# Performance work log

Measured on AMD Instinct MI355X. Metric: run time of the kernel, lower is better.

Reference implementation:

```python
import jax, jax.numpy as jnp
import numpy as np

D, H, F, Z = 768, 12, 2048, 100   # d_model, nhead, dim_feedforward, d_z
NL = 2                            # num enc layers == num dec layers
RATIO = 0.05                      # filter_ratio
EPS = 1e-5


def _ln(x, g, b):
    m = x.mean(-1, keepdims=True)
    v = ((x - m) ** 2).mean(-1, keepdims=True)
    return (x - m) / jnp.sqrt(v + EPS) * g + b


def _mha(x, bias, qkv_w, qkv_b, out_w, out_b):
    # x: [N, L, D] (torch seq-first: seq=N responses, batch=L token positions)
    # bias: [L, N] float key-padding mask, ADDED to logits (torch float-mask semantics)
    N, L, _ = x.shape
    hd = D // H
    qkv = jnp.einsum('nld,ed->nle', x, qkv_w) + qkv_b
    q, k, v = jnp.split(qkv, 3, axis=-1)
    q = q.reshape(N, L, H, hd)
    k = k.reshape(N, L, H, hd)
    v = v.reshape(N, L, H, hd)
    scores = jnp.einsum('nlhd,mlhd->lhnm', q, k) / jnp.sqrt(jnp.float32(hd))
    scores = scores + bias[:, None, None, :]
    attn = jax.nn.softmax(scores, axis=-1)
    o = jnp.einsum('lhnm,mlhd->nlhd', attn, v).reshape(N, L, D)
    return o @ out_w.T + out_b


def _stack(x, bias, p):
    qkv_w, qkv_b, out_w, out_b, g1, b1, w1, c1, w2, c2, g2, b2 = p
    for i in range(NL):  # post-norm TransformerEncoderLayer, relu FFN, eval (no dropout)
        a = _mha(x, bias, qkv_w[i], qkv_b[i], out_w[i], out_b[i])
        x = _ln(x + a, g1[i], b1[i])
        f = jax.nn.relu(x @ w1[i].T + c1[i]) @ w2[i].T + c2[i]
        x = _ln(x + f, g2[i], b2[i])
    return x


def _anomaly_scores(emb, msk, enc_p, dec_p, pe_w, pe_b, pd_w, pd_b):
    bias = msk.T  # [L, N]
    h = _stack(emb, bias, enc_p)
    z = jnp.tanh(h @ pe_w.T + pe_b)
    zd = jnp.tanh(z @ pd_w.T + pd_b)
    d = _stack(zd, bias, dec_p)
    # per-response MSE between mean decoded and mean input embedding, summed over D
    return ((d.mean(axis=1) - emb.mean(axis=1)) ** 2).sum(-1)


def _forward(tree_lens, inputs_embeds, attention_mask, enc_p, dec_p, pe_w, pe_b, pd_w, pd_b):
    B, T, L, _ = inputs_embeds.shape
    tls = np.asarray(tree_lens)
    n_resp = tls - 1
    # pack ragged replies: rows 1..tree_len-1 of every tree -> [Ntot, L, D]
    b_idx = np.concatenate([np.full(n, b) for b, n in enumerate(n_resp)])
    t_idx = np.concatenate([np.arange(1, tl) for tl in tls])
    reply = inputs_embeds[b_idx, t_idx]
    masks = attention_mask[b_idx, t_idx]
    s = _anomaly_scores(reply, masks, enc_p, dec_p, pe_w, pe_b, pd_w, pd_b)  # [Ntot]
    Ntot = s.shape[0]
    # original: rank_idx = global_argsort filtered to indices < n_resp[b] (min is always 0)
    # == argsort of the FIRST n_resp[b] packed scores (faithful to the source's indexing)
    masked = jnp.where(jnp.arange(Ntot)[None, :] < jnp.asarray(n_resp)[:, None],
                       s[None, :], jnp.inf)
    order = jnp.argsort(masked, axis=1)[:, :T - 1]  # [B, T-1]
    n_ext = np.maximum(np.floor(n_resp * RATIO).astype(np.int64), 1)
    sel = np.arange(T - 1)[None, :] < n_ext[:, None]          # [B, T-1]
    selj = jnp.asarray(sel)
    node_idx = jnp.where(selj, order + 1, 0)                  # pad slots reuse src (node 0)
    node_full = jnp.concatenate([jnp.zeros((B, 1), node_idx.dtype), node_idx], axis=1)
    brow = jnp.arange(B)[:, None]
    new_emb = inputs_embeds[brow, node_full]                  # [B, T, L, D]
    valid = jnp.asarray(np.concatenate([np.ones((B, 1), bool), sel], axis=1)
                        ).astype(attention_mask.dtype)
    new_msk = attention_mask[brow, node_full] * valid[:, :, None]  # pad rows get zero mask
    ohidx = jnp.where(selj, order + 1, T)                     # dump masked scatters to col T
    oh = jnp.zeros((B, T + 1), jnp.int32).at[brow, ohidx].set(1)[:, :T].at[:, 0].set(1)
    ext_mask = jnp.repeat(oh[:, :, None], L, axis=2).reshape(B, T * L)
    new_tree_lens = jnp.asarray(1 + n_ext, dtype=jnp.int32)
    n_ext_adv = 0
    return oh, ext_mask, n_ext_adv, new_tree_lens, new_emb, new_msk


def setup_inputs() -> dict:
    B, T, L = 16, 32, 64
    key = jax.random.key(0)
    ks = list(jax.random.split(key, 4))
    inp = {
        'tree_lens': jax.random.randint(ks[0], (B,), T // 2, T + 1),
        'inputs_embeds': jax.random.normal(ks[1], (B, T, L, D), jnp.float32),
        'attention_mask': jnp.ones((B, T, L), jnp.float32),
    }
    kit = iter(jax.random.split(ks[2], 32))
    def w(shape):
        return jax.random.normal(next(kit), (NL,) + shape, jnp.float32) * 0.02
    for pre in ('enc', 'dec'):
        inp[pre + '_qkv_w'] = w((3 * D, D)); inp[pre + '_qkv_b'] = jnp.zeros((NL, 3 * D))
        inp[pre + '_out_w'] = w((D, D));     inp[pre + '_out_b'] = jnp.zeros((NL, D))
        inp[pre + '_ln1_g'] = jnp.ones((NL, D)); inp[pre + '_ln1_b'] = jnp.zeros((NL, D))
        inp[pre + '_w1'] = w((F, D)); inp[pre + '_c1'] = jnp.zeros((NL, F))
        inp[pre + '_w2'] = w((D, F)); inp[pre + '_c2'] = jnp.zeros((NL, D))
        inp[pre + '_ln2_g'] = jnp.ones((NL, D)); inp[pre + '_ln2_b'] = jnp.zeros((NL, D))
    inp['pe_w'] = jax.random.normal(next(kit), (Z, D), jnp.float32) * 0.02
    inp['pe_b'] = jnp.zeros((Z,), jnp.float32)
    inp['pd_w'] = jax.random.normal(next(kit), (D, Z), jnp.float32) * 0.02
    inp['pd_b'] = jnp.zeros((D,), jnp.float32)
    return inp


def reference(tree_lens, inputs_embeds, attention_mask,
              enc_qkv_w, enc_qkv_b, enc_out_w, enc_out_b, enc_ln1_g, enc_ln1_b,
              enc_w1, enc_c1, enc_w2, enc_c2, enc_ln2_g, enc_ln2_b,
              dec_qkv_w, dec_qkv_b, dec_out_w, dec_out_b, dec_ln1_g, dec_ln1_b,
              dec_w1, dec_c1, dec_w2, dec_c2, dec_ln2_g, dec_ln2_b,
              pe_w, pe_b, pd_w, pd_b):
    enc_p = (enc_qkv_w, enc_qkv_b, enc_out_w, enc_out_b, enc_ln1_g, enc_ln1_b,
             enc_w1, enc_c1, enc_w2, enc_c2, enc_ln2_g, enc_ln2_b)
    dec_p = (dec_qkv_w, dec_qkv_b, dec_out_w, dec_out_b, dec_ln1_g, dec_ln1_b,
             dec_w1, dec_c1, dec_w2, dec_c2, dec_ln2_g, dec_ln2_b)
    return _forward(tree_lens, inputs_embeds, attention_mask, enc_p, dec_p,
                    pe_w, pe_b, pd_w, pd_b)
```

## Files before the change

kernel.cpp:

```cpp
#include <hip/hip_runtime.h>
#include <hip/hip_bf16.h>
#include <math.h>


#define B_  16
#define T_  32
#define L_  64
#define D_  768
#define H_  12
#define F_  2048
#define ZR_ 100
#define NP_ 512
#define EPS_ 1e-5f

#define MI_NTOT  0
#define MI_NRESP 8
#define MI_OFF   32
#define MI_BIDX  64
#define MI_TIDX  576
#define MI_NODE  1088

#define WS_BIAS2 2048
#define WS_EMEAN 34816
#define WS_S     428032
#define WS_WST   428544
#define WS_BIG   1313280

#define PEB_F    (WS_WST + 196608)

#define OUT_OH   0
#define OUT_EXT  512
#define OUT_NEA  33280
#define OUT_NTL  33281
#define OUT_NEMB 33297
#define OUT_NMSK 25199121
#define OUT_XSCR 33300
#define OUT_WSTK 12616224

#define WSEG0 1769472
#define WSEG1 589824
#define WSEG2 1572864
#define WSEG3 1572864
#define WPASS 5505024

typedef __attribute__((ext_vector_type(8))) short short8;
typedef __attribute__((ext_vector_type(4))) float f32x4;

__device__ inline float bf2f(unsigned s) {
  return __uint_as_float((s & 0xffffu) << 16);
}
__device__ inline unsigned short f2bf(float x) {
  unsigned u = __float_as_uint(x);
  u += 0x7fffu + ((u >> 16) & 1u);
  return (unsigned short)(u >> 16);
}
__device__ inline unsigned pack2(float a, float b) {
  return (unsigned)f2bf(a) | ((unsigned)f2bf(b) << 16);
}

__global__ void meta_kernel(const int* __restrict__ tl, int* __restrict__ mi) {
  if (threadIdx.x != 0) return;
  int off = 0;
  for (int b = 0; b < B_; b++) {
    int nr = tl[b] - 1;
    mi[MI_NRESP + b] = nr;
    mi[MI_OFF + b] = off;
    off += nr;
  }
  mi[MI_NTOT] = off;
  for (int j = 0; j < NP_; j++) {
    int b = -1, t = 0;
    if (j < off) {
      b = 0;
      while (b + 1 < B_ && j >= mi[MI_OFF + b + 1]) b++;
      t = j - mi[MI_OFF + b] + 1;
    }
    mi[MI_BIDX + j] = b;
    mi[MI_TIDX + j] = t;
  }
}

__global__ __launch_bounds__(256) void w2bf4_kernel(
    const float* __restrict__ s0, const float* __restrict__ s1,
    const float* __restrict__ s2, const float* __restrict__ s3,
    unsigned short* __restrict__ dst) {
  const int e = blockIdx.x * 1024 + threadIdx.x * 4;
  const float* src;
  int off;
  if (e < WSEG0)                         { src = s0; off = e; }
  else if (e < WSEG0 + WSEG1)            { src = s1; off = e - WSEG0; }
  else if (e < WSEG0 + WSEG1 + WSEG2)    { src = s2; off = e - WSEG0 - WSEG1; }
  else                                   { src = s3; off = e - WSEG0 - WSEG1 - WSEG2; }
  float4 v = *(const float4*)(src + off);
  uint2 pk; pk.x = pack2(v.x, v.y); pk.y = pack2(v.z, v.w);
  *(uint2*)(dst + e) = pk;
}

__global__ __launch_bounds__(256) void pepd_stage(
    const float* __restrict__ pew, const float* __restrict__ peb,
    const float* __restrict__ pdw,
    unsigned short* __restrict__ dpe, unsigned short* __restrict__ dpd,
    float* __restrict__ dpeb) {
  const int blk = blockIdx.x, t = threadIdx.x;
  if (blk < 192) {
    const int e = blk * 1024 + t * 4;
    const int r = e / 768, c = e % 768;
    float v[4];
    #pragma unroll
    for (int j = 0; j < 4; j++) v[j] = (r < ZR_) ? pew[r * 768 + c + j] : 0.f;
    uint2 pk; pk.x = pack2(v[0], v[1]); pk.y = pack2(v[2], v[3]);
    *(uint2*)(dpe + e) = pk;
  } else if (blk < 384) {
    const int e = (blk - 192) * 1024 + t * 4;
    const int r = e / 256, c = e % 256;
    float v[4];
    #pragma unroll
    for (int j = 0; j < 4; j++) v[j] = (c + j < ZR_) ? pdw[r * ZR_ + c + j] : 0.f;
    uint2 pk; pk.x = pack2(v[0], v[1]); pk.y = pack2(v[2], v[3]);
    *(uint2*)(dpd + e) = pk;
  } else {
    dpeb[t] = (t < ZR_) ? peb[t] : 0.f;
  }
}

__global__ __launch_bounds__(192) void gather_kernel(
    const float* __restrict__ emb, const float* __restrict__ am,
    const int* __restrict__ mi, unsigned short* __restrict__ X,
    float* __restrict__ bias2) {
  const int blk = blockIdx.x;
  const int j = blk >> 6, l = blk & 63;
  const int ntot = mi[MI_NTOT];
  const int t = threadIdx.x;
  float4 v = make_float4(0.f, 0.f, 0.f, 0.f);
  if (j < ntot) {
    const int b = mi[MI_BIDX + j], tt = mi[MI_TIDX + j];
    v = ((const float4*)(emb + (size_t)((b * T_ + tt) * L_ + l) * D_))[t];
    if (t == 0) bias2[blk] = am[(b * T_ + tt) * L_ + l];
  } else {
    if (t == 0) bias2[blk] = -1e30f;
  }
  uint2 pk; pk.x = pack2(v.x, v.y); pk.y = pack2(v.z, v.w);
  *(uint2*)(X + (size_t)blk * D_ + t * 4) = pk;
}

__global__ __launch_bounds__(256) void zerotail_kernel(const int* __restrict__ mi,
                                                       unsigned short* __restrict__ BIG) {
  const int row = blockIdx.x;
  if (row < mi[MI_NTOT] * 64) return;
  uint4 z = make_uint4(0u, 0u, 0u, 0u);
  uint4* p = (uint4*)(BIG + (size_t)row * 2304);
  for (int c = threadIdx.x; c < 288; c += 256) p[c] = z;
}

__global__ __launch_bounds__(256) void emean_kernel(const unsigned short* __restrict__ X,
                                                    float* __restrict__ em) {
  const int j = blockIdx.x;
  int d = threadIdx.x;
  for (int c = 0; c < 3; c++, d += 256) {
    const unsigned short* p = X + (size_t)j * L_ * D_ + d;
    float s = 0.f;
    for (int l = 0; l < L_; l++) s += bf2f(p[l * D_]);
    em[j * D_ + d] = s * (1.f / 64.f);
  }
}

__device__ inline float blockSum256(float v, float* red) {
  #pragma unroll
  for (int o = 32; o > 0; o >>= 1) v += __shfl_down(v, o);
  const int lane = threadIdx.x & 63, wid = threadIdx.x >> 6;
  __syncthreads();
  if (lane == 0) red[wid] = v;
  __syncthreads();
  return red[0] + red[1] + red[2] + red[3];
}

__global__ __launch_bounds__(256) void ln_kernel(unsigned short* __restrict__ X,
                                                 const float* __restrict__ g,
                                                 const float* __restrict__ bb,
                                                 const int* __restrict__ mi) {
  const int row = blockIdx.x;
  if (row >= mi[MI_NTOT] * L_) return;
  unsigned short* p = X + (size_t)row * D_;
  const int t = threadIdx.x;
  __shared__ float red[4];
  float v0 = bf2f(p[t]), v1 = bf2f(p[t + 256]), v2 = bf2f(p[t + 512]);
  float s = blockSum256(v0 + v1 + v2, red);
  float m = s * (1.f / 768.f);
  float d0 = v0 - m, d1 = v1 - m, d2 = v2 - m;
  float q = blockSum256(d0 * d0 + d1 * d1 + d2 * d2, red);
  float r = rsqrtf(q * (1.f / 768.f) + EPS_);
  p[t]       = f2bf(d0 * r * g[t]       + bb[t]);
  p[t + 256] = f2bf(d1 * r * g[t + 256] + bb[t + 256]);
  p[t + 512] = f2bf(d2 * r * g[t + 512] + bb[t + 512]);
}

template <int ACT, bool ADD>
__global__ __launch_bounds__(256, 2) void gemm_mfma(
    const unsigned short* __restrict__ A, int lda, int K,
    const unsigned short* __restrict__ W, int ldw,
    const float* __restrict__ bias,
    unsigned short* __restrict__ C, int ldc, int CT,
    const int* __restrict__ mi) {
  const int rows = mi[MI_NTOT] * 64;
  const int RTa = (rows + 255) >> 8;
  const int NTa = RTa * CT;
  const int id = blockIdx.x;
  if (id >= NTa) return;
  const int q8 = NTa >> 3, r8 = NTa & 7;
  const int xcd = id & 7, idx = id >> 3;
  const int wg = (xcd < r8 ? xcd * (q8 + 1) : r8 * (q8 + 1) + (xcd - r8) * q8) + idx;
  const int row0 = (wg / CT) * 256;
  const int col0 = (wg % CT) * 128;
  __shared__ unsigned short As[3][256 * 32];
  __shared__ unsigned short Bs[3][128 * 32];
  const int t = threadIdx.x;
  const int lane = t & 63, w = t >> 6;
  const int wr = w >> 1, wc = w & 1;
  const int quad = lane >> 4, l15 = lane & 15;

  const int srow = t >> 2;
  const int sgs = (t & 3) ^ ((t >> 3) & 3);
  const unsigned short* aSrc = A + (size_t)(row0 + srow) * lda + sgs * 8;
  const unsigned short* bSrc = W + (size_t)(col0 + srow) * ldw + sgs * 8;

#define STAGE_(kk, Ad, Bd)                                                      \
  do {                                                                          \
    __builtin_amdgcn_global_load_lds(                                           \
        (const __attribute__((address_space(1))) void*)(aSrc + (kk)),           \
        (__attribute__((address_space(3))) void*)((Ad) + w * 512), 16, 0, 0);   \
    __builtin_amdgcn_global_load_lds(                                           \
        (const __attribute__((address_space(1))) void*)(aSrc + (size_t)64 * lda + (kk)), \
        (__attribute__((address_space(3))) void*)((Ad) + 2048 + w * 512), 16, 0, 0); \
    __builtin_amdgcn_global_load_lds(                                           \
        (const __attribute__((address_space(1))) void*)(aSrc + (size_t)128 * lda + (kk)), \
        (__attribute__((address_space(3))) void*)((Ad) + 4096 + w * 512), 16, 0, 0); \
    __builtin_amdgcn_global_load_lds(                                           \
        (const __attribute__((address_space(1))) void*)(aSrc + (size_t)192 * lda + (kk)), \
        (__attribute__((address_space(3))) void*)((Ad) + 6144 + w * 512), 16, 0, 0); \
    __builtin_amdgcn_global_load_lds(                                           \
        (const __attribute__((address_space(1))) void*)(bSrc + (kk)),           \
        (__attribute__((address_space(3))) void*)((Bd) + w * 512), 16, 0, 0);   \
    __builtin_amdgcn_global_load_lds(                                           \
        (const __attribute__((address_space(1))) void*)(bSrc + (size_t)64 * ldw + (kk)), \
        (__attribute__((address_space(3))) void*)((Bd) + 2048 + w * 512), 16, 0, 0); \
  } while (0)

  auto LDA_ = [&](const unsigned short* buf, int m) -> short8 {
    const int ar = wr * 128 + m * 16 + l15;
    return *(const short8*)(buf + ar * 32 + (quad ^ ((ar >> 1) & 3)) * 8);
  };
  auto LDB_ = [&](const unsigned short* buf, int n) -> short8 {
    const int bn = wc * 64 + n * 16 + l15;
    return *(const short8*)(buf + bn * 32 + (quad ^ ((bn >> 1) & 3)) * 8);
  };

  f32x4 acc[8][4];
  #pragma unroll
  for (int m = 0; m < 8; m++)
    #pragma unroll
    for (int n = 0; n < 4; n++) acc[m][n] = (f32x4){0.f, 0.f, 0.f, 0.f};

  unsigned short* a0 = As[0]; unsigned short* a1 = As[1]; unsigned short* a2 = As[2];
  unsigned short* b0 = Bs[0]; unsigned short* b1 = Bs[1]; unsigned short* b2 = Bs[2];

  STAGE_(0, a0, b0);
  STAGE_(32, a1, b1);
  __builtin_amdgcn_sched_barrier(0);
  asm volatile("s_waitcnt vmcnt(6)" ::: "memory");
  __builtin_amdgcn_sched_barrier(0);
  __builtin_amdgcn_s_barrier();
  __builtin_amdgcn_sched_barrier(0);

  const int KT = K >> 5;
  for (int kt = 0; kt < KT; ++kt) {
    const bool m2 = (kt + 2) < KT;
    const int kn = (kt + 2) << 5;
    short8 afr[4], bfr[4];

    #pragma unroll
    for (int n = 0; n < 4; n++) bfr[n] = LDB_(b0, n);
    #pragma unroll
    for (int m = 0; m < 4; m++) afr[m] = LDA_(a0, m);
    if (m2) STAGE_(kn, a2, b2);
    __builtin_amdgcn_s_setprio(1);
    #pragma unroll
    for (int m = 0; m < 4; m++)
      #pragma unroll
      for (int n = 0; n < 4; n++)
        acc[m][n] = __builtin_amdgcn_mfma_f32_16x16x32_bf16(afr[m], bfr[n], acc[m][n], 0, 0, 0);
    __builtin_amdgcn_s_setprio(0);

    #pragma unroll
    for (int m = 0; m < 4; m++) afr[m] = LDA_(a0, m + 4);
    __builtin_amdgcn_s_setprio(1);
    #pragma unroll
    for (int m = 0; m < 4; m++)
      #pragma unroll
      for (int n = 0; n < 4; n++)
        acc[m + 4][n] = __builtin_amdgcn_mfma_f32_16x16x32_bf16(afr[m], bfr[n], acc[m + 4][n], 0, 0, 0);
    __builtin_amdgcn_s_setprio(0);

    if (kt + 1 < KT) {
      __builtin_amdgcn_sched_barrier(0);
      if (m2) asm volatile("s_waitcnt vmcnt(6)" ::: "memory");
      else    asm volatile("s_waitcnt vmcnt(0)" ::: "memory");
      __builtin_amdgcn_sched_barrier(0);
      __builtin_amdgcn_s_barrier();
      __builtin_amdgcn_sched_barrier(0);
    }
    unsigned short* ta = a0; a0 = a1; a1 = a2; a2 = ta;
    unsigned short* tb = b0; b0 = b1; b1 = b2; b2 = tb;
  }
#undef STAGE_

  float bv[4];
  #pragma unroll
  for (int n = 0; n < 4; n++) bv[n] = bias[col0 + wc * 64 + n * 16 + l15];
  #pragma unroll
  for (int m = 0; m < 8; m++) {
    #pragma unroll
    for (int reg = 0; reg < 4; reg++) {
      const size_t cr = (size_t)(row0 + wr * 128 + m * 16 + quad * 4 + reg) * ldc;
      #pragma unroll
      for (int n = 0; n < 4; n++) {
        const int cn = col0 + wc * 64 + n * 16 + l15;
        float x = acc[m][n][reg] + bv[n];
        if (ACT == 1) x = fmaxf(x, 0.f);
        if (ACT == 2) x = tanhf(x);
        if (ADD) x += bf2f(C[cr + cn]);
        C[cr + cn] = f2bf(x);
      }
    }
  }
}

__global__ __launch_bounds__(512) void attn_kernel(
    unsigned short* __restrict__ QKV, const float* __restrict__ bias2,
    const int* __restrict__ mi) {
  const int ntot = mi[MI_NTOT];
  const int id = blockIdx.x;
  const int xcd = id & 7, rr = id >> 3;
  const int ntp = rr & 3, lhi = rr >> 2;
  if (ntp * 128 >= ntot) return;
  const int lh = lhi * 8 + xcd;
  const int l = lh / H_, h = lh - l * H_;
  __shared__ unsigned short QPs[128 * 64];
  __shared__ unsigned short Ks0[64 * 64], Ks1[64 * 64];
  __shared__ unsigned short Vt0[64 * 64], Vt1[64 * 64];
  __shared__ float Bls[512];
  const int t = threadIdx.x;
  const int lane = t & 63, w = t >> 6;
  const int quad = lane >> 4, l15 = lane & 15;
  const int q0 = ntp * 128;
  const size_t TSTRIDE = (size_t)64 * L_ * 2304;

  const int krow = t >> 3;
  const int kgs = (t & 7) ^ (krow & 7);
  const unsigned short* ksrc =
      QKV + (size_t)(krow * L_ + l) * 2304 + 768 + h * 64 + kgs * 8;
  const unsigned short* vsrc =
      QKV + (size_t)(lane * L_ + l) * 2304 + 1536 + h * 64 + w * 8;

  auto stageK = [&](int mt, unsigned short* Kw) {
    __builtin_amdgcn_global_load_lds(
        (const __attribute__((address_space(1))) void*)(ksrc + (size_t)mt * TSTRIDE),
        (__attribute__((address_space(3))) void*)(Kw + w * 512), 16, 0, 0);
  };
  auto scatterV = [&](uint4 a0, unsigned short* Vw) {
    const unsigned short* p0 = (const unsigned short*)&a0;
    #pragma unroll
    for (int j = 0; j < 8; j++) {
      const int d = w * 8 + j;
      Vw[d * 64 + ((lane >> 3) ^ (d & 7)) * 8 + (lane & 7)] = p0[j];
    }
  };

  #pragma unroll
  for (int r = 0; r < 2; r++) {
    const int c = r * 512 + t;
    const int row = c >> 3, g = c & 7, gs = g ^ (row & 7);
    const unsigned short* gq =
        QKV + (size_t)((q0 + row) * L_ + l) * 2304 + h * 64 + gs * 8;
    __builtin_amdgcn_global_load_lds(
        (const __attribute__((address_space(1))) void*)gq,
        (__attribute__((address_space(3))) void*)(QPs + r * 4096 + w * 512), 16, 0, 0);
  }
  stageK(0, Ks0);
  uint4 pv0 = *(const uint4*)vsrc;
  Bls[t] = bias2[t * 64 + l];
  __syncthreads();

  const int qrow = w * 16 + l15;
  short8 aq[2];
  #pragma unroll
  for (int kq = 0; kq < 2; kq++)
    aq[kq] = *(const short8*)(QPs + qrow * 64 + ((kq * 4 + quad) ^ (qrow & 7)) * 8);
  scatterV(pv0, Vt0);
  __syncthreads();

  float runmax = -3.0e38f, runsum = 0.f;
  f32x4 oacc[4];
  #pragma unroll
  for (int i = 0; i < 4; i++) oacc[i] = (f32x4){0.f, 0.f, 0.f, 0.f};

  auto tilecomp = [&](int mt, const unsigned short* Krd, const unsigned short* Vrd) {
    f32x4 sa[4];
    #pragma unroll
    for (int n = 0; n < 4; n++) sa[n] = (f32x4){0.f, 0.f, 0.f, 0.f};
    __builtin_amdgcn_s_setprio(1);
    #pragma unroll
    for (int n = 0; n < 4; n++) {
      const int kr = n * 16 + l15;
      #pragma unroll
      for (int kq = 0; kq < 2; kq++) {
        const short8 bk = *(const short8*)(Krd + kr * 64 + ((kq * 4 + quad) ^ (kr & 7)) * 8);
        sa[n] = __builtin_amdgcn_mfma_f32_16x16x32_bf16(bk, aq[kq], sa[n], 0, 0, 0);
      }
    }
    __builtin_amdgcn_s_setprio(0);
    #pragma unroll
    for (int n = 0; n < 4; n++) {
      const float4 bj = *(const float4*)(Bls + mt * 64 + n * 16 + quad * 4);
      sa[n][0] = sa[n][0] * 0.125f + bj.x;
      sa[n][1] = sa[n][1] * 0.125f + bj.y;
      sa[n][2] = sa[n][2] * 0.125f + bj.z;
      sa[n][3] = sa[n][3] * 0.125f + bj.w;
    }

    float m16 = -3.0e38f;
    #pragma unroll
    for (int n = 0; n < 4; n++)
      m16 = fmaxf(m16, fmaxf(fmaxf(sa[n][0], sa[n][1]), fmaxf(sa[n][2], sa[n][3])));
    m16 = fmaxf(m16, __shfl_xor(m16, 16));
    m16 = fmaxf(m16, __shfl_xor(m16, 32));
    const float nm = fmaxf(runmax, m16);
    const float alpha = __expf(runmax - nm);
    runmax = nm;
    float s16 = 0.f;
    #pragma unroll
    for (int n = 0; n < 4; n++)
      #pragma unroll
      for (int reg = 0; reg < 4; reg++) {
        const float p = __expf(sa[n][reg] - nm);
        sa[n][reg] = p; s16 += p;
      }
    s16 += __shfl_xor(s16, 16);
    s16 += __shfl_xor(s16, 32);
    runsum = runsum * alpha + s16;
    float al[4];
    #pragma unroll
    for (int reg = 0; reg < 4; reg++)
      al[reg] = __shfl(alpha, (lane & 48) | (quad * 4 + reg));
    #pragma unroll
    for (int dn = 0; dn < 4; dn++)
      #pragma unroll
      for (int reg = 0; reg < 4; reg++) oacc[dn][reg] *= al[reg];

    #pragma unroll
    for (int n = 0; n < 4; n++)
      #pragma unroll
      for (int reg = 0; reg < 4; reg++) {
        const int key = n * 16 + quad * 4 + reg;
        QPs[qrow * 64 + ((key >> 3) ^ (qrow & 7)) * 8 + (key & 7)] = f2bf(sa[n][reg]);
      }
    short8 ap[2];
    #pragma unroll
    for (int kq = 0; kq < 2; kq++)
      ap[kq] = *(const short8*)(QPs + qrow * 64 + ((kq * 4 + quad) ^ (qrow & 7)) * 8);

    __builtin_amdgcn_s_setprio(1);
    #pragma unroll
    for (int dn = 0; dn < 4; dn++) {
      const int dr = dn * 16 + l15;
      #pragma unroll
      for (int kq = 0; kq < 2; kq++) {
        const short8 bv = *(const short8*)(Vrd + dr * 64 + ((kq * 4 + quad) ^ (dr & 7)) * 8);
        oacc[dn] = __builtin_amdgcn_mfma_f32_16x16x32_bf16(ap[kq], bv, oacc[dn], 0, 0, 0);
      }
    }
    __builtin_amdgcn_s_setprio(0);
  };

  for (int mt2 = 0; mt2 < 8; mt2 += 2) {
    {
      stageK(mt2 + 1, Ks1);
      uint4 n0 = *(const uint4*)(vsrc + (size_t)(mt2 + 1) * TSTRIDE);
      tilecomp(mt2, Ks0, Vt0);
      scatterV(n0, Vt1);
      __syncthreads();
    }
    {
      const bool more = (mt2 + 2) < 8;
      uint4 m0 = make_uint4(0, 0, 0, 0);
      if (more) {
        stageK(mt2 + 2, Ks0);
        m0 = *(const uint4*)(vsrc + (size_t)(mt2 + 2) * TSTRIDE);
      }
      tilecomp(mt2 + 1, Ks1, Vt1);
      if (more) scatterV(m0, Vt0);
      __syncthreads();
    }
  }

  const float inv = 1.f / runsum;
  float iv[4];
  #pragma unroll
  for (int reg = 0; reg < 4; reg++)
    iv[reg] = __shfl(inv, (lane & 48) | (quad * 4 + reg));
  #pragma unroll
  for (int reg = 0; reg < 4; reg++) {
    const int q = q0 + w * 16 + quad * 4 + reg;
    unsigned short* op = QKV + (size_t)(q * L_ + l) * 2304 + h * 64;
    #pragma unroll
    for (int dn = 0; dn < 4; dn++)
      op[dn * 16 + l15] = f2bf(oacc[dn][reg] * iv[reg]);
  }
}

__global__ __launch_bounds__(256) void score_kernel(const unsigned short* __restrict__ X,
                                                    const float* __restrict__ em,
                                                    float* __restrict__ Sv) {
  const int j = blockIdx.x;
  const int t = threadIdx.x;
  __shared__ float red[4];
  float part = 0.f;
  for (int c = 0; c < 3; c++) {
    const int d = t + c * 256;
    const unsigned short* p = X + (size_t)j * L_ * D_ + d;
    float s = 0.f;
    for (int l = 0; l < L_; l++) s += bf2f(p[l * D_]);
    const float diff = s * (1.f / 64.f) - em[j * D_ + d];
    part += diff * diff;
  }
  const float tot = blockSum256(part, red);
  if (t == 0) Sv[j] = tot;
}

__global__ __launch_bounds__(256) void finalize_kernel(const float* __restrict__ Sv,
                                                       int* __restrict__ mi,
                                                       float* __restrict__ out) {
  const int t = threadIdx.x;
  if (t < B_) {
    const int nr = mi[MI_NRESP + t];
    float best = 3.0e38f; int bi = 0;
    for (int j = 0; j < nr; j++) {
      const float v = Sv[j];
      if (v < best) { best = v; bi = j; }
    }
    mi[MI_NODE + t] = bi + 1;
    int next = nr / 20; if (next < 1) next = 1;
    out[OUT_NTL + t] = (float)(1 + next);
  }
  if (t == 0) out[OUT_NEA] = 0.f;
  __syncthreads();
  for (int idx = t; idx < B_ * T_; idx += 256) {
    const int b = idx >> 5, tt = idx & 31;
    out[OUT_OH + idx] = (tt == 0 || tt == mi[MI_NODE + b]) ? 1.f : 0.f;
  }
}

__global__ __launch_bounds__(256) void maskout_kernel(const float* __restrict__ am,
                                                      const int* __restrict__ mi,
                                                      float* __restrict__ out) {
  const int idx = blockIdx.x * 256 + threadIdx.x;
  const int b = idx >> 11, rem = idx & 2047;
  const int tt = rem >> 6, l = rem & 63;
  const int node = mi[MI_NODE + b];
  out[OUT_EXT + idx] = (tt == 0 || tt == node) ? 1.f : 0.f;
  float nm;
  if (tt == 0)      nm = am[(b * T_) * L_ + l];
  else if (tt == 1) nm = am[(b * T_ + node) * L_ + l];
  else              nm = 0.f;
  out[OUT_NMSK + idx] = nm;
}

__global__ __launch_bounds__(192) void newemb_kernel(const float* __restrict__ emb,
                                                     const int* __restrict__ mi,
                                                     float* __restrict__ out) {
  const int blk = blockIdx.x;
  const int b = blk >> 11, rem = blk & 2047;
  const int tt = rem >> 6, l = rem & 63;
  const int srct = (tt == 1) ? mi[MI_NODE + b] : 0;
  const float4 v = ((const float4*)(emb + (size_t)((b * T_ + srct) * L_ + l) * D_))[threadIdx.x];
  float* dst = out + OUT_NEMB + (size_t)blk * D_ + threadIdx.x * 4;
  dst[0] = v.x; dst[1] = v.y; dst[2] = v.z; dst[3] = v.w;
}

extern "C" void kernel_launch(void* const* d_in, const int* in_sizes, int n_in,
                              void* d_out, int out_size, void* d_ws, size_t ws_size,
                              hipStream_t stream) {
  (void)in_sizes; (void)n_in; (void)out_size; (void)ws_size;
  const int*   tl  = (const int*)d_in[0];
  const float* emb = (const float*)d_in[1];
  const float* am  = (const float*)d_in[2];
  const float* P[28];
  for (int i = 0; i < 28; i++) P[i] = (const float*)d_in[3 + i];

  float* wsf   = (float*)d_ws;
  int*   mi    = (int*)d_ws;
  float* bias2 = wsf + WS_BIAS2;
  float* emean = wsf + WS_EMEAN;
  float* Sv    = wsf + WS_S;
  unsigned short* Wst = (unsigned short*)(wsf + WS_WST);
  unsigned short* peW = Wst;
  unsigned short* pdW = Wst + 196608;
  float* peB   = wsf + PEB_F;
  unsigned short* BIG = (unsigned short*)(wsf + WS_BIG);
  unsigned short* Zs  = (unsigned short*)(wsf + WS_BIG);
  float* out   = (float*)d_out;
  unsigned short* X    = (unsigned short*)(out + OUT_XSCR);
  unsigned short* WSTK = (unsigned short*)(out + OUT_WSTK);

  meta_kernel<<<1, 64, 0, stream>>>(tl, mi);
  for (int p = 0; p < 4; p++) {
    const float* const* q = P + (p >> 1) * 12;
    const int i = p & 1;
    w2bf4_kernel<<<WPASS / 1024, 256, 0, stream>>>(
        q[0] + (size_t)i * 3 * D_ * D_, q[2] + (size_t)i * D_ * D_,
        q[6] + (size_t)i * F_ * D_, q[8] + (size_t)i * D_ * F_,
        WSTK + (size_t)p * WPASS);
  }
  pepd_stage<<<385, 256, 0, stream>>>(P[24], P[25], P[26], peW, pdW, peB);
  gather_kernel<<<NP_ * L_, 192, 0, stream>>>(emb, am, mi, X, bias2);
  emean_kernel<<<NP_, 256, 0, stream>>>(X, emean);
  zerotail_kernel<<<NP_ * L_, 256, 0, stream>>>(mi, BIG);

  const int RTM = 128;
  for (int s = 0; s < 2; s++) {
    const float* const* q = P + s * 12;
    for (int i = 0; i < 2; i++) {
      const unsigned short* WP = WSTK + (size_t)(s * 2 + i) * WPASS;
      gemm_mfma<0, false><<<RTM * 18, 256, 0, stream>>>(
          X, D_, D_, WP, D_, q[1] + i * 3 * D_, BIG, 3 * D_, 18, mi);
      attn_kernel<<<L_ * H_ * 4, 512, 0, stream>>>(BIG, bias2, mi);
      gemm_mfma<0, true><<<RTM * 6, 256, 0, stream>>>(
          BIG, 3 * D_, D_, WP + WSEG0, D_, q[3] + i * D_, X, D_, 6, mi);
      ln_kernel<<<NP_ * L_, 256, 0, stream>>>(X, q[4] + i * D_, q[5] + i * D_, mi);
      gemm_mfma<1, false><<<RTM * 16, 256, 0, stream>>>(
          X, D_, D_, WP + WSEG0 + WSEG1, D_, q[7] + i * F_, BIG, F_, 16, mi);
      gemm_mfma<0, true><<<RTM * 6, 256, 0, stream>>>(
          BIG, F_, F_, WP + WSEG0 + WSEG1 + WSEG2, F_, q[9] + i * D_, X, D_, 6, mi);
      ln_kernel<<<NP_ * L_, 256, 0, stream>>>(X, q[10] + i * D_, q[11] + i * D_, mi);
    }
    if (s == 0) {
      gemm_mfma<2, false><<<RTM * 2, 256, 0, stream>>>(
          X, D_, D_, peW, D_, peB, Zs, 256, 2, mi);
      gemm_mfma<2, false><<<RTM * 6, 256, 0, stream>>>(
          Zs, 256, 256, pdW, 256, P[27], X, D_, 6, mi);
    }
  }

  score_kernel<<<NP_, 256, 0, stream>>>(X, emean, Sv);
  finalize_kernel<<<1, 256, 0, stream>>>(Sv, mi, out);
  maskout_kernel<<<128, 256, 0, stream>>>(am, mi, out);
  newemb_kernel<<<B_ * T_ * L_, 192, 0, stream>>>(emb, mi, out);
}
```

Baseline: 2.661 ms.

## Split GEMM stage loads into halves interleaved with MFMA phases and barriers

```diff
diff --git a/kernel.cpp b/kernel.cpp
--- a/kernel.cpp
+++ b/kernel.cpp
@@ -223,26 +223,21 @@
   const unsigned short* aSrc = A + (size_t)(row0 + srow) * lda + sgs * 8;
   const unsigned short* bSrc = W + (size_t)(col0 + srow) * ldw + sgs * 8;
 
-#define STAGE_(kk, Ad, Bd)                                                      \
+#define GL_(src, dstbase)                                                       \
+  __builtin_amdgcn_global_load_lds(                                             \
+      (const __attribute__((address_space(1))) void*)(src),                     \
+      (__attribute__((address_space(3))) void*)(dstbase), 16, 0, 0)
+#define STAGE_H1_(kk, Ad, Bd)                                                   \
   do {                                                                          \
-    __builtin_amdgcn_global_load_lds(                                           \
-        (const __attribute__((address_space(1))) void*)(aSrc + (kk)),           \
-        (__attribute__((address_space(3))) void*)((Ad) + w * 512), 16, 0, 0);   \
-    __builtin_amdgcn_global_load_lds(                                           \
-        (const __attribute__((address_space(1))) void*)(aSrc + (size_t)64 * lda + (kk)), \
-        (__attribute__((address_space(3))) void*)((Ad) + 2048 + w * 512), 16, 0, 0); \
-    __builtin_amdgcn_global_load_lds(                                           \
-        (const __attribute__((address_space(1))) void*)(aSrc + (size_t)128 * lda + (kk)), \
-        (__attribute__((address_space(3))) void*)((Ad) + 4096 + w * 512), 16, 0, 0); \
-    __builtin_amdgcn_global_load_lds(                                           \
-        (const __attribute__((address_space(1))) void*)(aSrc + (size_t)192 * lda + (kk)), \
-        (__attribute__((address_space(3))) void*)((Ad) + 6144 + w * 512), 16, 0, 0); \
-    __builtin_amdgcn_global_load_lds(                                           \
-        (const __attribute__((address_space(1))) void*)(bSrc + (kk)),           \
-        (__attribute__((address_space(3))) void*)((Bd) + w * 512), 16, 0, 0);   \
-    __builtin_amdgcn_global_load_lds(                                           \
-        (const __attribute__((address_space(1))) void*)(bSrc + (size_t)64 * ldw + (kk)), \
-        (__attribute__((address_space(3))) void*)((Bd) + 2048 + w * 512), 16, 0, 0); \
+    GL_(aSrc + (kk),                        (Ad) + w * 512);                    \
+    GL_(aSrc + (size_t)64 * lda + (kk),     (Ad) + 2048 + w * 512);             \
+    GL_(bSrc + (kk),                        (Bd) + w * 512);                    \
+  } while (0)
+#define STAGE_H2_(kk, Ad, Bd)                                                   \
+  do {                                                                          \
+    GL_(aSrc + (size_t)128 * lda + (kk),    (Ad) + 4096 + w * 512);             \
+    GL_(aSrc + (size_t)192 * lda + (kk),    (Ad) + 6144 + w * 512);             \
+    GL_(bSrc + (size_t)64 * ldw + (kk),     (Bd) + 2048 + w * 512);             \
   } while (0)
 
   auto LDA_ = [&](const unsigned short* buf, int m) -> short8 {
@@ -260,11 +255,10 @@
     #pragma unroll
     for (int n = 0; n < 4; n++) acc[m][n] = (f32x4){0.f, 0.f, 0.f, 0.f};
 
-  unsigned short* a0 = As[0]; unsigned short* a1 = As[1]; unsigned short* a2 = As[2];
-  unsigned short* b0 = Bs[0]; unsigned short* b1 = Bs[1]; unsigned short* b2 = Bs[2];
-
-  STAGE_(0, a0, b0);
-  STAGE_(32, a1, b1);
+  STAGE_H1_(0, As[0], Bs[0]);
+  STAGE_H2_(0, As[0], Bs[0]);
+  STAGE_H1_(32, As[1], Bs[1]);
+  STAGE_H2_(32, As[1], Bs[1]);
   __builtin_amdgcn_sched_barrier(0);
   asm volatile("s_waitcnt vmcnt(6)" ::: "memory");
   __builtin_amdgcn_sched_barrier(0);
@@ -273,15 +267,21 @@
 
   const int KT = K >> 5;
   for (int kt = 0; kt < KT; ++kt) {
+    const unsigned short* Ac = As[kt % 3];
+    const unsigned short* Bc = Bs[kt % 3];
+    unsigned short* An = As[(kt + 2) % 3];
+    unsigned short* Bn = Bs[(kt + 2) % 3];
     const bool m2 = (kt + 2) < KT;
     const int kn = (kt + 2) << 5;
     short8 afr[4], bfr[4];
 
     #pragma unroll
-    for (int n = 0; n < 4; n++) bfr[n] = LDB_(b0, n);
-    #pragma unroll
-    for (int m = 0; m < 4; m++) afr[m] = LDA_(a0, m);
-    if (m2) STAGE_(kn, a2, b2);
+    for (int n = 0; n < 4; n++) bfr[n] = LDB_(Bc, n);
+    #pragma unroll
+    for (int m = 0; m < 4; m++) afr[m] = LDA_(Ac, m);
+    if (m2) STAGE_H1_(kn, An, Bn);
+    __builtin_amdgcn_sched_barrier(0);
+    __builtin_amdgcn_s_barrier();
     __builtin_amdgcn_s_setprio(1);
     #pragma unroll
     for (int m = 0; m < 4; m++)
@@ -289,29 +289,34 @@
       for (int n = 0; n < 4; n++)
         acc[m][n] = __builtin_amdgcn_mfma_f32_16x16x32_bf16(afr[m], bfr[n], acc[m][n], 0, 0, 0);
     __builtin_amdgcn_s_setprio(0);
-
-    #pragma unroll
-    for (int m = 0; m < 4; m++) afr[m] = LDA_(a0, m + 4);
-    __builtin_amdgcn_s_setprio(1);
-    #pragma unroll
-    for (int m = 0; m < 4; m++)
-      #pragma unroll
-      for (int n = 0; n < 4; n++)
-        acc[m + 4][n] = __builtin_amdgcn_mfma_f32_16x16x32_bf16(afr[m], bfr[n], acc[m + 4][n], 0, 0, 0);
-    __builtin_amdgcn_s_setprio(0);
-
+    __builtin_amdgcn_sched_barrier(0);
+    __builtin_amdgcn_s_barrier();
+    __builtin_amdgcn_sched_barrier(0);
+
+    #pragma unroll
+    for (int m = 0; m < 4; m++) afr[m] = LDA_(Ac, m + 4);
+    if (m2) STAGE_H2_(kn, An, Bn);
     if (kt + 1 < KT) {
       __builtin_amdgcn_sched_barrier(0);
       if (m2) asm volatile("s_waitcnt vmcnt(6)" ::: "memory");
       else    asm volatile("s_waitcnt vmcnt(0)" ::: "memory");
       __builtin_amdgcn_sched_barrier(0);
-      __builtin_amdgcn_s_barrier();
-      __builtin_amdgcn_sched_barrier(0);
-    }
-    unsigned short* ta = a0; a0 = a1; a1 = a2; a2 = ta;
-    unsigned short* tb = b0; b0 = b1; b1 = b2; b2 = tb;
-  }
-#undef STAGE_
+    }
+    __builtin_amdgcn_s_barrier();
+    __builtin_amdgcn_s_setprio(1);
+    #pragma unroll
+    for (int m = 0; m < 4; m++)
+      #pragma unroll
+      for (int n = 0; n < 4; n++)
+        acc[m + 4][n] = __builtin_amdgcn_mfma_f32_16x16x32_bf16(afr[m], bfr[n], acc[m + 4][n], 0, 0, 0);
+    __builtin_amdgcn_s_setprio(0);
+    __builtin_amdgcn_sched_barrier(0);
+    __builtin_amdgcn_s_barrier();
+    __builtin_amdgcn_sched_barrier(0);
+  }
+#undef STAGE_H1_
+#undef STAGE_H2_
+#undef GL_
 
   float bv[4];
   #pragma unroll
```

Result: slower. 2.788 ms (+4.8%).
